# Kernel optimization log

Hardware: AMD Instinct MI355X
Metric: run time of the kernel (lower is better)

Reference implementation:

```python
import jax, jax.numpy as jnp
import numpy as np

TEMPERATURE = 0.07
COS_EPS = 1e-8  # torch F.cosine_similarity clamps norms at eps=1e-8


def setup_inputs() -> dict:
    key = jax.random.key(0)
    features = jax.random.normal(key, (8192, 1024), dtype=jnp.float32)
    return {"features": features}


def reference(features):
    n = features.shape[0]
    b = n // 2
    # Cosine similarity as normalize + GEMM (equivalent to broadcasted F.cosine_similarity)
    norms = jnp.maximum(jnp.linalg.norm(features, axis=1, keepdims=True), COS_EPS)
    fn = features / norms                      # [N, D]
    sim = (fn @ fn.T) / TEMPERATURE            # [N, N]
    # Mask self-similarity on the diagonal with -inf
    diag = jnp.eye(n, dtype=bool)
    sim = jnp.where(diag, -jnp.inf, sim)
    # labels: positive of i is its paired augmentation (i+b mod n)
    labels = jnp.concatenate([jnp.arange(b) + b, jnp.arange(b)])  # [N]
    # Cross-entropy in one stable pass
    log_probs = jax.nn.log_softmax(sim, axis=1)
    loss = -jnp.mean(log_probs[jnp.arange(n), labels])
    return loss
```

## Files before the change

### kernel.cpp

```cpp
#include <hip/hip_runtime.h>
#include <hip/hip_bf16.h>

#define N_ROWS 8192
#define D_DIM  1024
#define HALF_N 4096
#define N_TILES 2080
#define N_RED  8
constexpr float INV_T = 1.0f / 0.07f;

typedef __attribute__((ext_vector_type(4)))  float f32x4;
typedef __attribute__((ext_vector_type(16))) float f32x16;
typedef __attribute__((ext_vector_type(4)))  int   i32x4;
typedef __attribute__((ext_vector_type(8)))  int   i32x8;

__device__ __forceinline__ void async_ld16(const void* g, void* lds) {
    __builtin_amdgcn_global_load_lds(
        (const __attribute__((address_space(1))) void*)g,
        (__attribute__((address_space(3))) void*)lds,
        16, 0, 0);
}

__device__ __forceinline__ unsigned int pk_fp8x4(float a, float b, float c, float d) {
    int v = __builtin_amdgcn_cvt_pk_fp8_f32(a, b, 0, false);
    v = __builtin_amdgcn_cvt_pk_fp8_f32(c, d, v, true);
    return (unsigned int)v;
}

__device__ __forceinline__ i32x8 ld_frag(const unsigned char* rowbase, int lo, int hi) {
    i32x4 L = *(const i32x4*)(rowbase + lo);
    i32x4 H = *(const i32x4*)(rowbase + hi);
    i32x8 r;
    r[0] = L[0]; r[1] = L[1]; r[2] = L[2]; r[3] = L[3];
    r[4] = H[0]; r[5] = H[1]; r[6] = H[2]; r[7] = H[3];
    return r;
}

#define MXMFMA(AF, BF, ACC) ACC = __builtin_amdgcn_mfma_scale_f32_32x32x64_f8f6f4( \
        AF, BF, ACC, 0, 0, 0, 0x7F7F7F7F, 0, 0x7F7F7F7F)

__global__ __launch_bounds__(256) void norm_kernel(const float* __restrict__ feat,
                                                   unsigned char* __restrict__ fn8,
                                                   float* __restrict__ row_sum,
                                                   unsigned int* __restrict__ done_cnt,
                                                   unsigned int* __restrict__ fin_cnt,
                                                   float* __restrict__ loss_acc) {
    const int w = threadIdx.x >> 6, lane = threadIdx.x & 63;
    const int row = blockIdx.x * 4 + w;
    if (blockIdx.x == 0 && threadIdx.x == 0) {
        *done_cnt = 0u;
        *fin_cnt = 0u;
        *loss_acc = 0.f;
    }
    const float4* src = (const float4*)(feat + (size_t)row * D_DIM);
    float4 v[4];
    float ss = 0.f;
#pragma unroll
    for (int t = 0; t < 4; ++t) {
        v[t] = src[lane + 64 * t];
        ss += v[t].x * v[t].x + v[t].y * v[t].y + v[t].z * v[t].z + v[t].w * v[t].w;
    }
#pragma unroll
    for (int off = 32; off; off >>= 1) ss += __shfl_xor(ss, off);
    float nrm = fmaxf(sqrtf(ss), 1e-8f);
    if (lane == 0) row_sum[row] = 0.f;
    const float inv = 1.0f / nrm;
    unsigned int* dst = (unsigned int*)(fn8 + (size_t)row * D_DIM);
#pragma unroll
    for (int t = 0; t < 4; ++t)
        dst[lane + 64 * t] = pk_fp8x4(v[t].x * inv, v[t].y * inv, v[t].z * inv, v[t].w * inv);
}

__global__ __launch_bounds__(256) void simgemm_kernel(const unsigned char* __restrict__ fn8,
                                                      float* __restrict__ row_sum,
                                                      float* __restrict__ s_target,
                                                      unsigned int* __restrict__ done_cnt,
                                                      unsigned int* __restrict__ fin_cnt,
                                                      float* __restrict__ loss_acc,
                                                      float* __restrict__ out) {
    __shared__ __align__(16) unsigned char As[128 * 128];
    __shared__ __align__(16) unsigned char Bs[128 * 128];
    const int t = blockIdx.x;
    int a = (int)((sqrtf(8.f * (float)t + 1.f) - 1.f) * 0.5f);
    while ((a + 1) * (a + 2) / 2 <= t) ++a;
    while (a * (a + 1) / 2 > t) --a;
    const int I = t - a * (a + 1) / 2;
    const int J = a;
    const int r0 = I * 128, c0 = J * 128;
    const bool isdiag = (I == J);
    const bool haspair = (J == I + 32);

    const int tid = threadIdx.x;
    const int w = tid >> 6, lane = tid & 63;
    const int wr = (w >> 1) * 64;
    const int wc = (w & 1) * 64;

    const int srow = lane >> 3;
    const int slog = ((lane & 7) ^ srow) * 16;
    const unsigned char* pa = fn8 + (size_t)(r0 + w * 32 + srow) * D_DIM + slog;
    const unsigned char* pb = fn8 + (size_t)(c0 + w * 32 + srow) * D_DIM + slog;

    const int fr = lane & 31;
    const int h = lane >> 5;
    const int fs = fr & 7;
    const unsigned char* pA0 = &As[(((w >> 1) * 2 + 0) * 4096) + fr * 128];
    const unsigned char* pA1 = &As[(((w >> 1) * 2 + 1) * 4096) + fr * 128];
    const unsigned char* pB0 = &Bs[(((w & 1) * 2 + 0) * 4096) + fr * 128];
    const unsigned char* pB1 = &Bs[(((w & 1) * 2 + 1) * 4096) + fr * 128];

    f32x16 acc[2][2] = {};

    for (int kt = 0; kt < 8; ++kt) {
        __syncthreads();
#pragma unroll
        for (int i = 0; i < 4; ++i) {
            async_ld16(pa + (size_t)i * 8 * D_DIM, &As[w * 4096 + i * 1024]);
            async_ld16(pb + (size_t)i * 8 * D_DIM, &Bs[w * 4096 + i * 1024]);
        }
        pa += 128; pb += 128;
        __syncthreads();

#pragma unroll
        for (int k64 = 0; k64 < 2; ++k64) {
            const int lo = ((4 * k64 + 2 * h) ^ fs) * 16;
            const int hi = ((4 * k64 + 2 * h + 1) ^ fs) * 16;
            i32x8 a0 = ld_frag(pA0, lo, hi);
            i32x8 a1 = ld_frag(pA1, lo, hi);
            i32x8 b0 = ld_frag(pB0, lo, hi);
            i32x8 b1 = ld_frag(pB1, lo, hi);
            MXMFMA(a0, b0, acc[0][0]);
            MXMFMA(a0, b1, acc[0][1]);
            MXMFMA(a1, b0, acc[1][0]);
            MXMFMA(a1, b1, acc[1][1]);
        }
    }

    const int colL = lane & 31;
    float cs[2] = {0.f, 0.f};
#pragma unroll
    for (int ti = 0; ti < 2; ++ti) {
#pragma unroll
        for (int reg = 0; reg < 16; ++reg) {
            const int rowL = (reg & 3) + 8 * (reg >> 2) + 4 * h;
            const int grow = r0 + wr + ti * 32 + rowL;
            float s = 0.f;
#pragma unroll
            for (int tj = 0; tj < 2; ++tj) {
                const int gcol = c0 + wc + tj * 32 + colL;
                float sim = acc[ti][tj][reg] * INV_T;
                float e = __expf(sim - INV_T);
                if (isdiag && grow == gcol) e = 0.f;
                if (haspair && gcol == grow + HALF_N) {
                    __hip_atomic_store(&s_target[grow], sim, __ATOMIC_RELAXED,
                                       __HIP_MEMORY_SCOPE_AGENT);
                    __hip_atomic_store(&s_target[gcol], sim, __ATOMIC_RELAXED,
                                       __HIP_MEMORY_SCOPE_AGENT);
                }
                s += e;
                cs[tj] += e;
            }
            s += __shfl_xor(s, 1);
            s += __shfl_xor(s, 2);
            s += __shfl_xor(s, 4);
            s += __shfl_xor(s, 8);
            s += __shfl_xor(s, 16);
            if (colL == 0) atomicAdd(&row_sum[grow], s);
        }
    }
    if (!isdiag) {
#pragma unroll
        for (int tj = 0; tj < 2; ++tj) {
            float s = cs[tj] + __shfl_xor(cs[tj], 32);
            if (h == 0) atomicAdd(&row_sum[c0 + wc + tj * 32 + colL], s);
        }
    }

    __syncthreads();
    __shared__ unsigned int my_ord;
    if (tid == 0)
        my_ord = __hip_atomic_fetch_add(done_cnt, 1u, __ATOMIC_RELAXED,
                                        __HIP_MEMORY_SCOPE_AGENT);
    __syncthreads();
    const unsigned int ord = my_ord;
    if (ord >= N_TILES - N_RED) {
        if (tid == 0) {
            while (__hip_atomic_load(done_cnt, __ATOMIC_RELAXED,
                                     __HIP_MEMORY_SCOPE_AGENT) < N_TILES)
                __builtin_amdgcn_s_sleep(1);
        }
        __syncthreads();
        const int slice = (int)(ord - (N_TILES - N_RED));
        const int base_row = slice * (N_ROWS / N_RED) + tid * 4;
        float rv[4], sv[4];
#pragma unroll
        for (int u = 0; u < 4; ++u) {
            rv[u] = __hip_atomic_load(&row_sum[base_row + u], __ATOMIC_RELAXED,
                                      __HIP_MEMORY_SCOPE_AGENT);
            sv[u] = __hip_atomic_load(&s_target[base_row + u], __ATOMIC_RELAXED,
                                      __HIP_MEMORY_SCOPE_AGENT);
        }
        float local = 0.f;
#pragma unroll
        for (int u = 0; u < 4; ++u)
            local += __logf(rv[u]) - sv[u];
#pragma unroll
        for (int off = 32; off; off >>= 1) local += __shfl_xor(local, off);
        __shared__ float part[4];
        if ((tid & 63) == 0) part[tid >> 6] = local;
        __syncthreads();
        if (tid == 0) {
            float bsum = part[0] + part[1] + part[2] + part[3];
            __hip_atomic_fetch_add(loss_acc, bsum, __ATOMIC_RELAXED,
                                   __HIP_MEMORY_SCOPE_AGENT);
            unsigned int f = __hip_atomic_fetch_add(fin_cnt, 1u, __ATOMIC_ACQ_REL,
                                                    __HIP_MEMORY_SCOPE_AGENT);
            if (f == N_RED - 1) {
                float accv = __hip_atomic_load(loss_acc, __ATOMIC_RELAXED,
                                               __HIP_MEMORY_SCOPE_AGENT);
                out[0] = INV_T + accv * (1.0f / N_ROWS);
            }
        }
    }
}

extern "C" void kernel_launch(void* const* d_in, const int* in_sizes, int n_in,
                              void* d_out, int out_size, void* d_ws, size_t ws_size,
                              hipStream_t stream) {
    const float* feat = (const float*)d_in[0];
    float* out = (float*)d_out;
    char* ws = (char*)d_ws;

    unsigned char* fn8 = (unsigned char*)ws;
    size_t off = (size_t)N_ROWS * D_DIM;
    float* row_sum = (float*)(ws + off);   off += N_ROWS * sizeof(float);
    float* s_target = (float*)(ws + off);  off += N_ROWS * sizeof(float);
    unsigned int* done_cnt = (unsigned int*)(ws + off);  off += sizeof(unsigned int);
    unsigned int* fin_cnt = (unsigned int*)(ws + off);   off += sizeof(unsigned int);
    float* loss_acc = (float*)(ws + off);

    norm_kernel<<<N_ROWS / 4, 256, 0, stream>>>(feat, fn8, row_sum, done_cnt, fin_cnt, loss_acc);
    simgemm_kernel<<<N_TILES, 256, 0, stream>>>(fn8, row_sum, s_target, done_cnt, fin_cnt, loss_acc, out);
}
```

Before: 148.6 us.

## Double-buffer LDS tiles with async prefetch and a new swizzle layout

Measured after the change: 211.3 us. +42.2%, slower.

```diff
diff --git a/kernel.cpp b/kernel.cpp
--- a/kernel.cpp
+++ b/kernel.cpp
@@ -26,9 +26,9 @@
     return (unsigned int)v;
 }
 
-__device__ __forceinline__ i32x8 ld_frag(const unsigned char* rowbase, int lo, int hi) {
-    i32x4 L = *(const i32x4*)(rowbase + lo);
-    i32x4 H = *(const i32x4*)(rowbase + hi);
+__device__ __forceinline__ i32x8 ld_frag(const unsigned char* p, int lo) {
+    i32x4 L = *(const i32x4*)(p + lo);
+    i32x4 H = *(const i32x4*)(p + (lo ^ 16));
     i32x8 r;
     r[0] = L[0]; r[1] = L[1]; r[2] = L[2]; r[3] = L[3];
     r[4] = H[0]; r[5] = H[1]; r[6] = H[2]; r[7] = H[3];
@@ -70,6 +70,10 @@
         dst[lane + 64 * t] = pk_fp8x4(v[t].x * inv, v[t].y * inv, v[t].z * inv, v[t].w * inv);
 }
 
+#define BARRIER() do { asm volatile("" ::: "memory"); \
+    __builtin_amdgcn_s_barrier();                      \
+    asm volatile("" ::: "memory"); } while (0)
+
 __global__ __launch_bounds__(256) void simgemm_kernel(const unsigned char* __restrict__ fn8,
                                                       float* __restrict__ row_sum,
                                                       float* __restrict__ s_target,
@@ -77,8 +81,8 @@
                                                       unsigned int* __restrict__ fin_cnt,
                                                       float* __restrict__ loss_acc,
                                                       float* __restrict__ out) {
-    __shared__ __align__(16) unsigned char As[128 * 128];
-    __shared__ __align__(16) unsigned char Bs[128 * 128];
+    __shared__ __align__(16) unsigned char As[2][16 * 1024];
+    __shared__ __align__(16) unsigned char Bs[2][16 * 1024];
     const int t = blockIdx.x;
     int a = (int)((sqrtf(8.f * (float)t + 1.f) - 1.f) * 0.5f);
     while ((a + 1) * (a + 2) / 2 <= t) ++a;
@@ -94,44 +98,65 @@
     const int wr = (w >> 1) * 64;
     const int wc = (w & 1) * 64;
 
-    const int srow = lane >> 3;
-    const int slog = ((lane & 7) ^ srow) * 16;
-    const unsigned char* pa = fn8 + (size_t)(r0 + w * 32 + srow) * D_DIM + slog;
-    const unsigned char* pb = fn8 + (size_t)(c0 + w * 32 + srow) * D_DIM + slog;
+    const int srow2 = lane >> 2;
+    const int slog2 = (((lane & 3) ^ ((lane >> 3) & 3))) * 16;
+    const unsigned char* pA[4];
+    const unsigned char* pB[4];
+#pragma unroll
+    for (int c = 0; c < 4; ++c) {
+        const size_t roff = (size_t)(w * 32 + (c & 1) * 16 + srow2) * D_DIM
+                            + (c >> 1) * 64 + slog2;
+        pA[c] = fn8 + (size_t)r0 * D_DIM + roff;
+        pB[c] = fn8 + (size_t)c0 * D_DIM + roff;
+    }
 
     const int fr = lane & 31;
     const int h = lane >> 5;
-    const int fs = fr & 7;
-    const unsigned char* pA0 = &As[(((w >> 1) * 2 + 0) * 4096) + fr * 128];
-    const unsigned char* pA1 = &As[(((w >> 1) * 2 + 1) * 4096) + fr * 128];
-    const unsigned char* pB0 = &Bs[(((w & 1) * 2 + 0) * 4096) + fr * 128];
-    const unsigned char* pB1 = &Bs[(((w & 1) * 2 + 1) * 4096) + fr * 128];
+    const int fkey = (fr >> 1) & 3;
+    const int ca0 = ((w >> 1) * 2 + 0) * 4096 + fr * 64;
+    const int ca1 = ((w >> 1) * 2 + 1) * 4096 + fr * 64;
+    const int cb0 = ((w & 1) * 2 + 0) * 4096 + fr * 64;
+    const int cb1 = ((w & 1) * 2 + 1) * 4096 + fr * 64;
 
     f32x16 acc[2][2] = {};
 
+#pragma unroll
+    for (int c = 0; c < 4; ++c) {
+        async_ld16(pA[c], &As[0][w * 4096 + c * 1024]);
+        async_ld16(pB[c], &Bs[0][w * 4096 + c * 1024]);
+    }
+    asm volatile("s_waitcnt vmcnt(0)" ::: "memory");
+    BARRIER();
+
+    int buf = 0;
     for (int kt = 0; kt < 8; ++kt) {
-        __syncthreads();
-#pragma unroll
-        for (int i = 0; i < 4; ++i) {
-            async_ld16(pa + (size_t)i * 8 * D_DIM, &As[w * 4096 + i * 1024]);
-            async_ld16(pb + (size_t)i * 8 * D_DIM, &Bs[w * 4096 + i * 1024]);
-        }
-        pa += 128; pb += 128;
-        __syncthreads();
-
+        if (kt < 7) {
+            const int koff = (kt + 1) * 128;
+#pragma unroll
+            for (int c = 0; c < 4; ++c) {
+                async_ld16(pA[c] + koff, &As[buf ^ 1][w * 4096 + c * 1024]);
+                async_ld16(pB[c] + koff, &Bs[buf ^ 1][w * 4096 + c * 1024]);
+            }
+        }
+        const unsigned char* bA = &As[buf][0];
+        const unsigned char* bB = &Bs[buf][0];
 #pragma unroll
         for (int k64 = 0; k64 < 2; ++k64) {
-            const int lo = ((4 * k64 + 2 * h) ^ fs) * 16;
-            const int hi = ((4 * k64 + 2 * h + 1) ^ fs) * 16;
-            i32x8 a0 = ld_frag(pA0, lo, hi);
-            i32x8 a1 = ld_frag(pA1, lo, hi);
-            i32x8 b0 = ld_frag(pB0, lo, hi);
-            i32x8 b1 = ld_frag(pB1, lo, hi);
+            const int lo = k64 * 2048 + ((2 * h) ^ fkey) * 16;
+            i32x8 a0 = ld_frag(bA + ca0, lo);
+            i32x8 a1 = ld_frag(bA + ca1, lo);
+            i32x8 b0 = ld_frag(bB + cb0, lo);
+            i32x8 b1 = ld_frag(bB + cb1, lo);
             MXMFMA(a0, b0, acc[0][0]);
             MXMFMA(a0, b1, acc[0][1]);
             MXMFMA(a1, b0, acc[1][0]);
             MXMFMA(a1, b1, acc[1][1]);
         }
+        if (kt < 7) {
+            asm volatile("s_waitcnt vmcnt(0)" ::: "memory");
+            BARRIER();
+        }
+        buf ^= 1;
     }
 
     const int colL = lane & 31;
```

## Double-buffer LDS tiles to overlap global loads with MFMA compute

Applied to the files above, without the earlier changes.

Result: slower. 169.8 us (+14.2%).

```diff
diff --git a/kernel.cpp b/kernel.cpp
--- a/kernel.cpp
+++ b/kernel.cpp
@@ -70,6 +70,10 @@
         dst[lane + 64 * t] = pk_fp8x4(v[t].x * inv, v[t].y * inv, v[t].z * inv, v[t].w * inv);
 }
 
+#define BARRIER() do { asm volatile("" ::: "memory"); \
+    __builtin_amdgcn_s_barrier();                      \
+    asm volatile("" ::: "memory"); } while (0)
+
 __global__ __launch_bounds__(256) void simgemm_kernel(const unsigned char* __restrict__ fn8,
                                                       float* __restrict__ row_sum,
                                                       float* __restrict__ s_target,
@@ -77,8 +81,8 @@
                                                       unsigned int* __restrict__ fin_cnt,
                                                       float* __restrict__ loss_acc,
                                                       float* __restrict__ out) {
-    __shared__ __align__(16) unsigned char As[128 * 128];
-    __shared__ __align__(16) unsigned char Bs[128 * 128];
+    __shared__ __align__(16) unsigned char As[2][16 * 1024];
+    __shared__ __align__(16) unsigned char Bs[2][16 * 1024];
     const int t = blockIdx.x;
     int a = (int)((sqrtf(8.f * (float)t + 1.f) - 1.f) * 0.5f);
     while ((a + 1) * (a + 2) / 2 <= t) ++a;
@@ -102,36 +106,55 @@
     const int fr = lane & 31;
     const int h = lane >> 5;
     const int fs = fr & 7;
-    const unsigned char* pA0 = &As[(((w >> 1) * 2 + 0) * 4096) + fr * 128];
-    const unsigned char* pA1 = &As[(((w >> 1) * 2 + 1) * 4096) + fr * 128];
-    const unsigned char* pB0 = &Bs[(((w & 1) * 2 + 0) * 4096) + fr * 128];
-    const unsigned char* pB1 = &Bs[(((w & 1) * 2 + 1) * 4096) + fr * 128];
+    const int ca0 = (((w >> 1) * 2 + 0) * 4096) + fr * 128;
+    const int ca1 = (((w >> 1) * 2 + 1) * 4096) + fr * 128;
+    const int cb0 = (((w & 1) * 2 + 0) * 4096) + fr * 128;
+    const int cb1 = (((w & 1) * 2 + 1) * 4096) + fr * 128;
 
     f32x16 acc[2][2] = {};
 
+#pragma unroll
+    for (int i = 0; i < 4; ++i) {
+        async_ld16(pa + (size_t)i * 8 * D_DIM, &As[0][w * 4096 + i * 1024]);
+        async_ld16(pb + (size_t)i * 8 * D_DIM, &Bs[0][w * 4096 + i * 1024]);
+    }
+    pa += 128; pb += 128;
+    asm volatile("s_waitcnt vmcnt(0)" ::: "memory");
+    BARRIER();
+
+    int buf = 0;
+#pragma unroll 1
     for (int kt = 0; kt < 8; ++kt) {
-        __syncthreads();
-#pragma unroll
-        for (int i = 0; i < 4; ++i) {
-            async_ld16(pa + (size_t)i * 8 * D_DIM, &As[w * 4096 + i * 1024]);
-            async_ld16(pb + (size_t)i * 8 * D_DIM, &Bs[w * 4096 + i * 1024]);
-        }
-        pa += 128; pb += 128;
-        __syncthreads();
-
+        if (kt < 7) {
+#pragma unroll
+            for (int i = 0; i < 4; ++i) {
+                async_ld16(pa + (size_t)i * 8 * D_DIM, &As[buf ^ 1][w * 4096 + i * 1024]);
+                async_ld16(pb + (size_t)i * 8 * D_DIM, &Bs[buf ^ 1][w * 4096 + i * 1024]);
+            }
+            pa += 128; pb += 128;
+        }
+        const unsigned char* bA = &As[buf][0];
+        const unsigned char* bB = &Bs[buf][0];
 #pragma unroll
         for (int k64 = 0; k64 < 2; ++k64) {
             const int lo = ((4 * k64 + 2 * h) ^ fs) * 16;
             const int hi = ((4 * k64 + 2 * h + 1) ^ fs) * 16;
-            i32x8 a0 = ld_frag(pA0, lo, hi);
-            i32x8 a1 = ld_frag(pA1, lo, hi);
-            i32x8 b0 = ld_frag(pB0, lo, hi);
-            i32x8 b1 = ld_frag(pB1, lo, hi);
+            i32x8 a0 = ld_frag(bA + ca0, lo, hi);
+            i32x8 a1 = ld_frag(bA + ca1, lo, hi);
+            i32x8 b0 = ld_frag(bB + cb0, lo, hi);
+            i32x8 b1 = ld_frag(bB + cb1, lo, hi);
+            __builtin_amdgcn_s_setprio(1);
             MXMFMA(a0, b0, acc[0][0]);
             MXMFMA(a0, b1, acc[0][1]);
             MXMFMA(a1, b0, acc[1][0]);
             MXMFMA(a1, b1, acc[1][1]);
-        }
+            __builtin_amdgcn_s_setprio(0);
+        }
+        if (kt < 7) {
+            asm volatile("s_waitcnt vmcnt(0)" ::: "memory");
+            BARRIER();
+        }
+        buf ^= 1;
     }
 
     const int colL = lane & 31;
```

## Load GEMM fragments directly from global memory, dropping LDS staging

Applied to the files above, without the earlier changes.

Result: slower. 218.3 us (+46.9%).

```diff
diff --git a/kernel.cpp b/kernel.cpp
--- a/kernel.cpp
+++ b/kernel.cpp
@@ -13,22 +13,15 @@
 typedef __attribute__((ext_vector_type(4)))  int   i32x4;
 typedef __attribute__((ext_vector_type(8)))  int   i32x8;
 
-__device__ __forceinline__ void async_ld16(const void* g, void* lds) {
-    __builtin_amdgcn_global_load_lds(
-        (const __attribute__((address_space(1))) void*)g,
-        (__attribute__((address_space(3))) void*)lds,
-        16, 0, 0);
-}
-
 __device__ __forceinline__ unsigned int pk_fp8x4(float a, float b, float c, float d) {
     int v = __builtin_amdgcn_cvt_pk_fp8_f32(a, b, 0, false);
     v = __builtin_amdgcn_cvt_pk_fp8_f32(c, d, v, true);
     return (unsigned int)v;
 }
 
-__device__ __forceinline__ i32x8 ld_frag(const unsigned char* rowbase, int lo, int hi) {
-    i32x4 L = *(const i32x4*)(rowbase + lo);
-    i32x4 H = *(const i32x4*)(rowbase + hi);
+__device__ __forceinline__ i32x8 ld_g32(const unsigned char* p) {
+    i32x4 L = *(const i32x4*)p;
+    i32x4 H = *(const i32x4*)(p + 16);
     i32x8 r;
     r[0] = L[0]; r[1] = L[1]; r[2] = L[2]; r[3] = L[3];
     r[4] = H[0]; r[5] = H[1]; r[6] = H[2]; r[7] = H[3];
@@ -70,15 +63,13 @@
         dst[lane + 64 * t] = pk_fp8x4(v[t].x * inv, v[t].y * inv, v[t].z * inv, v[t].w * inv);
 }
 
-__global__ __launch_bounds__(256) void simgemm_kernel(const unsigned char* __restrict__ fn8,
-                                                      float* __restrict__ row_sum,
-                                                      float* __restrict__ s_target,
-                                                      unsigned int* __restrict__ done_cnt,
-                                                      unsigned int* __restrict__ fin_cnt,
-                                                      float* __restrict__ loss_acc,
-                                                      float* __restrict__ out) {
-    __shared__ __align__(16) unsigned char As[128 * 128];
-    __shared__ __align__(16) unsigned char Bs[128 * 128];
+__global__ __launch_bounds__(256, 4) void simgemm_kernel(const unsigned char* __restrict__ fn8,
+                                                         float* __restrict__ row_sum,
+                                                         float* __restrict__ s_target,
+                                                         unsigned int* __restrict__ done_cnt,
+                                                         unsigned int* __restrict__ fin_cnt,
+                                                         float* __restrict__ loss_acc,
+                                                         float* __restrict__ out) {
     const int t = blockIdx.x;
     int a = (int)((sqrtf(8.f * (float)t + 1.f) - 1.f) * 0.5f);
     while ((a + 1) * (a + 2) / 2 <= t) ++a;
@@ -94,44 +85,28 @@
     const int wr = (w >> 1) * 64;
     const int wc = (w & 1) * 64;
 
-    const int srow = lane >> 3;
-    const int slog = ((lane & 7) ^ srow) * 16;
-    const unsigned char* pa = fn8 + (size_t)(r0 + w * 32 + srow) * D_DIM + slog;
-    const unsigned char* pb = fn8 + (size_t)(c0 + w * 32 + srow) * D_DIM + slog;
-
     const int fr = lane & 31;
     const int h = lane >> 5;
-    const int fs = fr & 7;
-    const unsigned char* pA0 = &As[(((w >> 1) * 2 + 0) * 4096) + fr * 128];
-    const unsigned char* pA1 = &As[(((w >> 1) * 2 + 1) * 4096) + fr * 128];
-    const unsigned char* pB0 = &Bs[(((w & 1) * 2 + 0) * 4096) + fr * 128];
-    const unsigned char* pB1 = &Bs[(((w & 1) * 2 + 1) * 4096) + fr * 128];
+    const unsigned char* gA0 = fn8 + (size_t)(r0 + wr + 0  + fr) * D_DIM + h * 32;
+    const unsigned char* gA1 = fn8 + (size_t)(r0 + wr + 32 + fr) * D_DIM + h * 32;
+    const unsigned char* gB0 = fn8 + (size_t)(c0 + wc + 0  + fr) * D_DIM + h * 32;
+    const unsigned char* gB1 = fn8 + (size_t)(c0 + wc + 32 + fr) * D_DIM + h * 32;
 
     f32x16 acc[2][2] = {};
 
-    for (int kt = 0; kt < 8; ++kt) {
-        __syncthreads();
-#pragma unroll
-        for (int i = 0; i < 4; ++i) {
-            async_ld16(pa + (size_t)i * 8 * D_DIM, &As[w * 4096 + i * 1024]);
-            async_ld16(pb + (size_t)i * 8 * D_DIM, &Bs[w * 4096 + i * 1024]);
-        }
-        pa += 128; pb += 128;
-        __syncthreads();
-
-#pragma unroll
-        for (int k64 = 0; k64 < 2; ++k64) {
-            const int lo = ((4 * k64 + 2 * h) ^ fs) * 16;
-            const int hi = ((4 * k64 + 2 * h + 1) ^ fs) * 16;
-            i32x8 a0 = ld_frag(pA0, lo, hi);
-            i32x8 a1 = ld_frag(pA1, lo, hi);
-            i32x8 b0 = ld_frag(pB0, lo, hi);
-            i32x8 b1 = ld_frag(pB1, lo, hi);
-            MXMFMA(a0, b0, acc[0][0]);
-            MXMFMA(a0, b1, acc[0][1]);
-            MXMFMA(a1, b0, acc[1][0]);
-            MXMFMA(a1, b1, acc[1][1]);
-        }
+#pragma unroll 1
+    for (int kk = 0; kk < 16; ++kk) {
+        const int ko = kk * 64;
+        i32x8 a0 = ld_g32(gA0 + ko);
+        i32x8 a1 = ld_g32(gA1 + ko);
+        i32x8 b0 = ld_g32(gB0 + ko);
+        i32x8 b1 = ld_g32(gB1 + ko);
+        __builtin_amdgcn_s_setprio(1);
+        MXMFMA(a0, b0, acc[0][0]);
+        MXMFMA(a0, b1, acc[0][1]);
+        MXMFMA(a1, b0, acc[1][0]);
+        MXMFMA(a1, b1, acc[1][1]);
+        __builtin_amdgcn_s_setprio(0);
     }
 
     const int colL = lane & 31;
```
